# Kernel optimization log

Hardware: AMD Instinct MI355X
Metric: run time of the kernel (lower is better)

The kernel has to match this reference:

```python
import jax, jax.numpy as jnp
import numpy as np

HEADS = 16
HEAD_DIM = 64
NEG = 1000000000.0  # additive mask magnitude from source


def setup_inputs() -> dict:
    key = jax.random.key(0)
    ks = jax.random.split(key, 6)
    N, S, D = 4, 2048, 1024
    x = jax.random.normal(ks[0], (N, S, D), dtype=jnp.float32)
    scale = 1.0 / np.sqrt(D)
    wq = jax.random.normal(ks[1], (D, D), dtype=jnp.float32) * scale
    wk = jax.random.normal(ks[2], (D, D), dtype=jnp.float32) * scale
    wv = jax.random.normal(ks[3], (D, D), dtype=jnp.float32) * scale
    wo = jax.random.normal(ks[4], (D, D), dtype=jnp.float32) * scale
    bo = jnp.zeros((D,), dtype=jnp.float32)
    return {"x": x, "wq": wq, "wk": wk, "wv": wv, "wo": wo, "bo": bo}


def reference(x, wq, wk, wv, wo, bo):
    N, S, D = x.shape
    h, d = HEADS, HEAD_DIM
    attn_scale = 1.0 / np.sqrt(d)
    # projections (no bias, qkv_bias=False)
    q = (x @ wq.T).reshape(N, S, h, d).transpose(0, 2, 1, 3)  # N h S d
    k = (x @ wk.T).reshape(N, S, h, d).transpose(0, 2, 1, 3)  # N h S d
    v = (x @ wv.T).reshape(N, S, h, d).transpose(0, 2, 1, 3)  # N h S d
    logits = jnp.einsum('nhsd,nhtd->nhst', q, k) * attn_scale  # N h S S
    scores = jax.nn.softmax(logits, axis=-1)
    # faithful quirk: additive mask applied AFTER softmax
    # triu(ones) - 1 -> 0 on/above diagonal, -1 strictly below
    causal_mask = NEG * (jnp.triu(jnp.ones((S, S), dtype=x.dtype)) - 1.0)
    scores = scores + causal_mask  # broadcasts over N, h
    out = jnp.einsum('nhst,nhtd->nhsd', scores, v)  # N h S d
    out = out.transpose(0, 2, 1, 3).reshape(N, S, h * d)
    return out @ wo.T + bo  # dropout p=0 -> identity
```

## Files before the change

### kernel.cpp

```cpp
#include <hip/hip_runtime.h>

#define AS1 __attribute__((address_space(1)))
#define AS3 __attribute__((address_space(3)))

typedef __bf16 bf16x8 __attribute__((ext_vector_type(8)));
typedef float f32x4 __attribute__((ext_vector_type(4)));

__device__ __forceinline__ unsigned short f2bf(float f) {
  unsigned int u = __float_as_uint(f);
  return (unsigned short)((u + 0x7fffu + ((u >> 16) & 1u)) >> 16);
}

__device__ __forceinline__ void gemm_body(int bx, int by, int bz,
                                          const unsigned short* __restrict__ A,
                                          const unsigned short* __restrict__ B,
                                          float* __restrict__ C,
                                          const float* __restrict__ bias,
                                          int ldC, int K, int kchunk, int planeElems,
                                          unsigned short* lA, unsigned short* lB) {
  int tid = threadIdx.x;
  int w = tid >> 6, lane = tid & 63;
  int r0 = bx * 128, c0 = by * 128;
  int wr = w >> 1, wc = w & 1;
  int ml = lane & 15, q = lane >> 4;
  C += (size_t)bz * planeElems;

  int srow = lane >> 3;
  int scol = 8 * ((lane & 7) ^ srow);
  const unsigned short* gA = A + (size_t)(r0 + 32 * w + srow) * K + scol + (size_t)bz * kchunk;
  const unsigned short* gB = B + (size_t)(c0 + 32 * w + srow) * K + scol + (size_t)bz * kchunk;
  unsigned short* lApw = lA + 32 * w * 64;
  unsigned short* lBpw = lB + 32 * w * 64;

  const f32x4 vzero = {0.f, 0.f, 0.f, 0.f};
  f32x4 acc[4][4];
#pragma unroll
  for (int mt = 0; mt < 4; ++mt)
#pragma unroll
    for (int nt = 0; nt < 4; ++nt) acc[mt][nt] = vzero;

  for (int k0 = 0; k0 < kchunk; k0 += 64) {
#pragma unroll
    for (int n = 0; n < 4; ++n) {
      __builtin_amdgcn_global_load_lds((const AS1 void*)(gA + (size_t)8 * n * K + k0),
                                       (AS3 void*)(lApw + n * 512), 16, 0, 0);
      __builtin_amdgcn_global_load_lds((const AS1 void*)(gB + (size_t)8 * n * K + k0),
                                       (AS3 void*)(lBpw + n * 512), 16, 0, 0);
    }
    __syncthreads();
#pragma unroll
    for (int h = 0; h < 2; ++h) {
      bf16x8 af[4], bfv[4];
      int kb = 4 * h + q;
#pragma unroll
      for (int mt = 0; mt < 4; ++mt) {
        int R = 64 * wr + 16 * mt + ml;
        af[mt] = *(const bf16x8*)(lA + R * 64 + 8 * (kb ^ (ml & 7)));
      }
#pragma unroll
      for (int nt = 0; nt < 4; ++nt) {
        int R = 64 * wc + 16 * nt + ml;
        bfv[nt] = *(const bf16x8*)(lB + R * 64 + 8 * (kb ^ (ml & 7)));
      }
#pragma unroll
      for (int mt = 0; mt < 4; ++mt)
#pragma unroll
        for (int nt = 0; nt < 4; ++nt)
          acc[mt][nt] = __builtin_amdgcn_mfma_f32_16x16x32_bf16(af[mt], bfv[nt], acc[mt][nt], 0, 0, 0);
    }
    __syncthreads();
  }

#pragma unroll
  for (int nt = 0; nt < 4; ++nt) {
    int col = c0 + 64 * wc + 16 * nt + ml;
    float bv = bias ? bias[col] : 0.f;
#pragma unroll
    for (int mt = 0; mt < 4; ++mt) {
      int rowb = r0 + 64 * wr + 16 * mt + q * 4;
#pragma unroll
      for (int r = 0; r < 4; ++r)
        C[(size_t)(rowb + r) * ldC + col] = acc[mt][nt][r] + bv;
    }
  }
}

__global__ __launch_bounds__(256) void prep_tilesum_k(const float* __restrict__ x,
                                                      const float* __restrict__ wo,
                                                      const float* __restrict__ wv,
                                                      float* __restrict__ T,
                                                      unsigned short* __restrict__ wo_b,
                                                      unsigned short* __restrict__ wvT_b) {
  __shared__ float t[32][33];
  int b = blockIdx.x;
  if (b < 512) {
    int bt = b >> 2;
    int f = (b & 3) * 256 + threadIdx.x;
    const float* p = x + (size_t)bt * 65536 + f;
    float s = 0.f;
#pragma unroll 8
    for (int i = 0; i < 64; ++i) s += p[(size_t)i * 1024];
    T[(size_t)bt * 1024 + f] = s;
  } else if (b < 1536) {
    int i = ((b - 512) * 256 + threadIdx.x) * 4;
    float4 v = *(const float4*)(wo + i);
    ushort4 o;
    o.x = f2bf(v.x); o.y = f2bf(v.y); o.z = f2bf(v.z); o.w = f2bf(v.w);
    *(ushort4*)(wo_b + i) = o;
  } else {
    int bb = b - 1536;
    int bx = (bb & 31) * 32, by = (bb >> 5) * 32;
    int tx = threadIdx.x & 31, ty = threadIdx.x >> 5;
    for (int i = ty; i < 32; i += 8) t[i][tx] = wv[(by + i) * 1024 + bx + tx];
    __syncthreads();
    for (int i = ty; i < 32; i += 8) wvT_b[(bx + i) * 1024 + by + tx] = f2bf(t[tx][i]);
  }
}

__global__ __launch_bounds__(256) void scan_smallgemm_k(const float* __restrict__ x,
                                                        const float* __restrict__ T,
                                                        unsigned short* __restrict__ Xc,
                                                        const unsigned short* __restrict__ wo_b,
                                                        const unsigned short* __restrict__ wvT_b,
                                                        float* __restrict__ Pf) {
  __shared__ unsigned short lA[128 * 64];
  __shared__ unsigned short lB[128 * 64];
  int b = blockIdx.x;
  if (b < 512) {
    int bt = b >> 2;
    int tile = bt & 31, b0 = bt - tile;
    int f = (b & 3) * 256 + threadIdx.x;
    float acc = 0.f;
    for (int t = 0; t < tile; ++t) acc += T[(size_t)(b0 + t) * 1024 + f];
    const float* px = x + (size_t)bt * 65536 + f;
    unsigned short* po = Xc + (size_t)bt * 65536 + f;
#pragma unroll 4
    for (int i = 0; i < 64; ++i) {
      po[(size_t)i * 1024] = f2bf(acc);
      acc += px[(size_t)i * 1024];
    }
  } else {
    int g = b - 512;
    gemm_body(g & 7, (g >> 3) & 7, g >> 6, wo_b, wvT_b, Pf, nullptr,
              1024, 1024, 256, 1 << 20, lA, lB);
  }
}

__global__ __launch_bounds__(256) void reduce_cast_k(const float* __restrict__ P,
                                                     unsigned short* __restrict__ Mp) {
  int i = (blockIdx.x * 256 + threadIdx.x) * 4;
  float4 a = *(const float4*)(P + i);
  float4 b = *(const float4*)(P + (1u << 20) + i);
  float4 c = *(const float4*)(P + (2u << 20) + i);
  float4 d = *(const float4*)(P + (3u << 20) + i);
  ushort4 o;
  o.x = f2bf(-1e9f * (a.x + b.x + c.x + d.x));
  o.y = f2bf(-1e9f * (a.y + b.y + c.y + d.y));
  o.z = f2bf(-1e9f * (a.z + b.z + c.z + d.z));
  o.w = f2bf(-1e9f * (a.w + b.w + c.w + d.w));
  *(ushort4*)(Mp + i) = o;
}

__global__ __launch_bounds__(256) void gemm_big_k(const unsigned short* __restrict__ A,
                                                  const unsigned short* __restrict__ B,
                                                  float* __restrict__ C,
                                                  const float* __restrict__ bias) {
  __shared__ unsigned short lA[128 * 64];
  __shared__ unsigned short lB[128 * 64];
  gemm_body(blockIdx.x, blockIdx.y, 0, A, B, C, bias, 1024, 1024, 1024, 0, lA, lB);
}

extern "C" void kernel_launch(void* const* d_in, const int* in_sizes, int n_in,
                              void* d_out, int out_size, void* d_ws, size_t ws_size,
                              hipStream_t stream) {
  const float* x  = (const float*)d_in[0];
  const float* wv = (const float*)d_in[3];
  const float* wo = (const float*)d_in[4];
  const float* bo = (const float*)d_in[5];
  char* ws = (char*)d_ws;

  unsigned short* wo_b  = (unsigned short*)ws;
  unsigned short* wvT_b = (unsigned short*)(ws + (2u << 20));
  unsigned short* Mp    = (unsigned short*)(ws + (4u << 20));
  float*          Tsum  = (float*)(ws + (6u << 20));
  unsigned short* Xc    = (unsigned short*)(ws + (7u << 20));
  float*          Pf    = (float*)(ws + (23u << 20));

  prep_tilesum_k<<<2560, 256, 0, stream>>>(x, wo, wv, Tsum, wo_b, wvT_b);
  scan_smallgemm_k<<<768, 256, 0, stream>>>(x, Tsum, Xc, wo_b, wvT_b, Pf);
  reduce_cast_k<<<1024, 256, 0, stream>>>(Pf, Mp);
  gemm_big_k<<<dim3(64, 8), 256, 0, stream>>>(Xc, Mp, (float*)d_out, bo);
}
```

Before: 146.1 us.

## Vectorize tile-sum/scan with float2, reorder blocks, and remap GEMM grid

The tile-sum and prefix-scan sections now process two adjacent features per thread using float2 loads and packed bf16 stores, halving their block counts. In the scan kernel the GEMM blocks move ahead of the scan blocks so the heavier MFMA work is dispatched first. The big GEMM switches to a 1D grid with a remapped block index so consecutive blocks share B tiles (column-major order over row tiles), aimed at better L2 reuse. Fewer threads in the scan path reduce parallelism over the sequential column scan.

```diff
diff --git a/kernel.cpp b/kernel.cpp
--- a/kernel.cpp
+++ b/kernel.cpp
@@ -93,22 +93,26 @@
                                                       unsigned short* __restrict__ wvT_b) {
   __shared__ float t[32][33];
   int b = blockIdx.x;
-  if (b < 512) {
-    int bt = b >> 2;
-    int f = (b & 3) * 256 + threadIdx.x;
+  if (b < 256) {
+    int bt = b >> 1;
+    int f = (b & 1) * 512 + threadIdx.x * 2;
     const float* p = x + (size_t)bt * 65536 + f;
-    float s = 0.f;
+    float sx = 0.f, sy = 0.f;
 #pragma unroll 8
-    for (int i = 0; i < 64; ++i) s += p[(size_t)i * 1024];
-    T[(size_t)bt * 1024 + f] = s;
-  } else if (b < 1536) {
-    int i = ((b - 512) * 256 + threadIdx.x) * 4;
+    for (int i = 0; i < 64; ++i) {
+      float2 v = *(const float2*)(p + (size_t)i * 1024);
+      sx += v.x; sy += v.y;
+    }
+    float2 s = {sx, sy};
+    *(float2*)(T + (size_t)bt * 1024 + f) = s;
+  } else if (b < 1280) {
+    int i = ((b - 256) * 256 + threadIdx.x) * 4;
     float4 v = *(const float4*)(wo + i);
     ushort4 o;
     o.x = f2bf(v.x); o.y = f2bf(v.y); o.z = f2bf(v.z); o.w = f2bf(v.w);
     *(ushort4*)(wo_b + i) = o;
   } else {
-    int bb = b - 1536;
+    int bb = b - 1280;
     int bx = (bb & 31) * 32, by = (bb >> 5) * 32;
     int tx = threadIdx.x & 31, ty = threadIdx.x >> 5;
     for (int i = ty; i < 32; i += 8) t[i][tx] = wv[(by + i) * 1024 + bx + tx];
@@ -126,23 +130,29 @@
   __shared__ unsigned short lA[128 * 64];
   __shared__ unsigned short lB[128 * 64];
   int b = blockIdx.x;
-  if (b < 512) {
-    int bt = b >> 2;
+  if (b < 256) {
+    int g = b;
+    gemm_body(g & 7, (g >> 3) & 7, g >> 6, wo_b, wvT_b, Pf, nullptr,
+              1024, 1024, 256, 1 << 20, lA, lB);
+  } else {
+    int sb = b - 256;
+    int bt = sb >> 1;
     int tile = bt & 31, b0 = bt - tile;
-    int f = (b & 3) * 256 + threadIdx.x;
-    float acc = 0.f;
-    for (int t = 0; t < tile; ++t) acc += T[(size_t)(b0 + t) * 1024 + f];
+    int f = (sb & 1) * 512 + threadIdx.x * 2;
+    float ax = 0.f, ay = 0.f;
+    for (int t = 0; t < tile; ++t) {
+      float2 v = *(const float2*)(T + (size_t)(b0 + t) * 1024 + f);
+      ax += v.x; ay += v.y;
+    }
     const float* px = x + (size_t)bt * 65536 + f;
     unsigned short* po = Xc + (size_t)bt * 65536 + f;
 #pragma unroll 4
     for (int i = 0; i < 64; ++i) {
-      po[(size_t)i * 1024] = f2bf(acc);
-      acc += px[(size_t)i * 1024];
-    }
-  } else {
-    int g = b - 512;
-    gemm_body(g & 7, (g >> 3) & 7, g >> 6, wo_b, wvT_b, Pf, nullptr,
-              1024, 1024, 256, 1 << 20, lA, lB);
+      unsigned int pk = (unsigned int)f2bf(ax) | ((unsigned int)f2bf(ay) << 16);
+      *(unsigned int*)(po + (size_t)i * 1024) = pk;
+      float2 v = *(const float2*)(px + (size_t)i * 1024);
+      ax += v.x; ay += v.y;
+    }
   }
 }
 
@@ -167,7 +177,9 @@
                                                   const float* __restrict__ bias) {
   __shared__ unsigned short lA[128 * 64];
   __shared__ unsigned short lB[128 * 64];
-  gemm_body(blockIdx.x, blockIdx.y, 0, A, B, C, bias, 1024, 1024, 1024, 0, lA, lB);
+  int p = blockIdx.x;
+  int l = (p & 7) * 64 + (p >> 3);
+  gemm_body(l >> 3, l & 7, 0, A, B, C, bias, 1024, 1024, 1024, 0, lA, lB);
 }
 
 extern "C" void kernel_launch(void* const* d_in, const int* in_sizes, int n_in,
@@ -186,8 +198,8 @@
   unsigned short* Xc    = (unsigned short*)(ws + (7u << 20));
   float*          Pf    = (float*)(ws + (23u << 20));
 
-  prep_tilesum_k<<<2560, 256, 0, stream>>>(x, wo, wv, Tsum, wo_b, wvT_b);
-  scan_smallgemm_k<<<768, 256, 0, stream>>>(x, Tsum, Xc, wo_b, wvT_b, Pf);
+  prep_tilesum_k<<<2304, 256, 0, stream>>>(x, wo, wv, Tsum, wo_b, wvT_b);
+  scan_smallgemm_k<<<512, 256, 0, stream>>>(x, Tsum, Xc, wo_b, wvT_b, Pf);
   reduce_cast_k<<<1024, 256, 0, stream>>>(Pf, Mp);
-  gemm_big_k<<<dim3(64, 8), 256, 0, stream>>>(Xc, Mp, (float*)d_out, bo);
-}
+  gemm_big_k<<<512, 256, 0, stream>>>(Xc, Mp, (float*)d_out, bo);
+}
```

New measurement: 143.7 us. Within noise of the previous version (-1.7%).
